# Kernel optimization log

Measured on AMD Instinct MI355X. Metric: run time of the kernel, lower is better.

## Reference

```python
import jax, jax.numpy as jnp
import numpy as np

G, N = 1024, 40            # graphs, nodes per graph (complete graphs)
SLOPE = 0.1                # leaky relu negative slope
SMAT_IDX = jnp.array([0, 1, 2, 3, 1, 4, 5, 6, 2, 5, 7, 8, 3, 6, 8, 9])


def setup_inputs() -> dict:
    key = jax.random.key(0)
    ks = jax.random.split(key, 24)

    # --- graph structure: G identical complete graphs of N nodes ---
    ii, jj = np.meshgrid(np.arange(N), np.arange(N), indexing="ij")
    mask = ii != jj
    src_l, dst_l = ii[mask], jj[mask]              # directed edges per graph
    offs = (np.arange(G) * N)[:, None]
    edge_index = np.stack([(src_l[None] + offs).ravel(),
                           (dst_l[None] + offs).ravel()]).astype(np.int64)
    iu, ju = np.triu_indices(N, 1)
    M = iu.shape[0]                                 # 780 undirected edges
    ud_edges = np.stack([iu, ju], 1).astype(np.int64)
    edge_map = np.zeros((N, N), np.int64)
    edge_map[iu, ju] = np.arange(M)
    edge_map[ju, iu] = np.arange(M)

    def w(k, shape, fan_in):
        return jax.random.normal(k, shape, jnp.float32) / np.sqrt(fan_in)

    inp = {
        "x": jax.random.normal(ks[0], (G * N, 16), jnp.float32),
        "edge_index": jnp.asarray(edge_index),
        "ud_edges": jnp.asarray(ud_edges),
        "edge_map": jnp.asarray(edge_map),
        # GCN stack 6->32->32->64
        "Wg0": w(ks[1], (6, 32), 6),   "bg0": jnp.zeros((32,), jnp.float32),
        "Wg1": w(ks[2], (32, 32), 32), "bg1": jnp.zeros((32,), jnp.float32),
        "Wg2": w(ks[3], (32, 64), 32), "bg2": jnp.zeros((64,), jnp.float32),
        # node MLP 64->64->64->10
        "Wn0": w(ks[4], (64, 64), 64), "bn0": jnp.zeros((64,), jnp.float32),
        "Wn1": w(ks[5], (64, 64), 64), "bn1": jnp.zeros((64,), jnp.float32),
        "Wn2": w(ks[6], (64, 10), 64), "bn2": jnp.zeros((10,), jnp.float32),
        # edge MLP 64->64->64->10
        "We0": w(ks[7], (64, 64), 64), "be0": jnp.zeros((64,), jnp.float32),
        "We1": w(ks[8], (64, 64), 64), "be1": jnp.zeros((64,), jnp.float32),
        "We2": w(ks[9], (64, 10), 64), "be2": jnp.zeros((10,), jnp.float32),
    }
    return inp


def _forward(x, edge_index, ud_edges, edge_map,
             Wg0, bg0, Wg1, bg1, Wg2, bg2,
             Wn0, bn0, Wn1, bn1, Wn2, bn2,
             We0, be0, We1, be1, We2, be2):
    num_nodes = x.shape[0]
    h = x[:, :6]                                   # node_feature_mode == 1
    src, dst = edge_index[0], edge_index[1]

    # GCN normalization (add_self_loops=False, edge_weight=1)
    deg = jax.ops.segment_sum(jnp.ones(src.shape[0], x.dtype), dst,
                              num_segments=num_nodes)
    dis = jnp.where(deg > 0, jax.lax.rsqrt(jnp.maximum(deg, 1e-12)), 0.0)
    norm = dis[src] * dis[dst]                     # [E]

    def gcn(h, W, b):
        m = (h @ W)[src] * norm[:, None]
        return jax.ops.segment_sum(m, dst, num_segments=num_nodes) + b

    # eval mode: dropout is identity
    h = jax.nn.leaky_relu(gcn(h, Wg0, bg0), SLOPE)
    h = jax.nn.leaky_relu(gcn(h, Wg1, bg1), SLOPE)
    h = gcn(h, Wg2, bg2)                           # [G*N, 64]

    hg = h.reshape(G, N, -1)                       # [G, N, 64]

    def mlp(z, Ws, bs):
        for W, b in zip(Ws[:-1], bs[:-1]):
            z = jax.nn.leaky_relu(z @ W + b, SLOPE)
        return z @ Ws[-1] + bs[-1]

    vp = mlp(hg, [Wn0, Wn1, Wn2], [bn0, bn1, bn2])            # [G, N, 10]
    e = hg[:, ud_edges[:, 0], :] + hg[:, ud_edges[:, 1], :]   # [G, M, 64]
    ep = mlp(e, [We0, We1, We2], [be0, be1, be2])             # [G, M, 10]

    # recover_X: diag blocks smat(vp[i]), off-diag smat(ep[edge_map[i,j]])
    epm = ep[:, edge_map, :]                                  # [G, N, N, 10]
    eye = jnp.eye(N, dtype=bool)[None, :, :, None]
    vecs = jnp.where(eye, vp[:, :, None, :], epm)             # [G, N, N, 10]
    blocks = vecs[..., SMAT_IDX].reshape(G, N, N, 4, 4)
    X = blocks.transpose(0, 1, 3, 2, 4).reshape(G, 4 * N, 4 * N)
    return h, X


def reference(x, edge_index, ud_edges, edge_map,
              Wg0, bg0, Wg1, bg1, Wg2, bg2,
              Wn0, bn0, Wn1, bn1, Wn2, bn2,
              We0, be0, We1, be1, We2, be2):
    return _forward(x, edge_index, ud_edges, edge_map,
                    Wg0, bg0, Wg1, bg1, Wg2, bg2,
                    Wn0, bn0, Wn1, bn1, Wn2, bn2,
                    We0, be0, We1, be1, We2, be2)
```

## Files before the change

kernel.cpp:

```cpp
#include <hip/hip_runtime.h>

#define G_GRAPHS 1024
#define N_NODES  40
#define M_EDGES  780
#define NUM_NODES (G_GRAPHS * N_NODES)
#define H_ELEMS  (NUM_NODES * 64)
#define X_STRIDE 160
#define X_PER_G  25600
#define SLOPE 0.1f

#define PACK_PER_MLP 9216

typedef __bf16 bf16x8 __attribute__((ext_vector_type(8)));
typedef unsigned short us8 __attribute__((ext_vector_type(8)));
typedef float f32x4 __attribute__((ext_vector_type(4)));

__device__ __forceinline__ float lrelu(float v) { return fmaxf(v, SLOPE * v); }
__device__ __forceinline__ unsigned short f2bf(float x) {
    __bf16 b = (__bf16)x;
    return __builtin_bit_cast(unsigned short, b);
}
__device__ __forceinline__ unsigned int pk2bf(float a, float b) {
    return (unsigned int)f2bf(a) | ((unsigned int)f2bf(b) << 16);
}

__global__ __launch_bounds__(256) void k_prep(const float* __restrict__ We0,
                                              const float* __restrict__ We1,
                                              const float* __restrict__ We2,
                                              const float* __restrict__ Wn0,
                                              const float* __restrict__ Wn1,
                                              const float* __restrict__ Wn2,
                                              unsigned short* __restrict__ wp) {
    int t = blockIdx.x * 256 + threadIdx.x;
    int mlp = t / PACK_PER_MLP;
    int o = t - mlp * PACK_PER_MLP;
    const float* W0 = mlp ? Wn0 : We0;
    const float* W1 = mlp ? Wn1 : We1;
    const float* W2 = mlp ? Wn2 : We2;
    float val;
    if (o < 8192) {
        const float* W = (o < 4096) ? W0 : W1;
        int idx = o & 4095;
        int j = idx & 7, l = (idx >> 3) & 63, tt = idx >> 9;
        int kt = tt & 1, mt = tt >> 1;
        int k = kt * 32 + ((l >> 4) & 3) * 8 + j;
        int m = mt * 16 + (l & 15);
        val = W[k * 64 + m];
    } else {
        int idx = o - 8192;
        int j = idx & 7, l = (idx >> 3) & 63, kt = idx >> 9;
        int k = kt * 32 + ((l >> 4) & 3) * 8 + j;
        int m = l & 15;
        val = (m < 10) ? W2[k * 10 + m] : 0.f;
    }
    wp[mlp * PACK_PER_MLP + o] = f2bf(val);
}

struct ChunkRegs {
    bf16x8 A1[4][2];
    bf16x8 A2[4][2];
    bf16x8 A3[2];
    float4 bv0[4];
    float4 bv1[4];
    float  bz[4];
};

__device__ __forceinline__ void run_pair(int R0A, int R0B, int w, int l,
                                         const float4* sh4,
                                         unsigned short* sBA,
                                         unsigned short* sBB,
                                         float* sEP,
                                         const ChunkRegs& cr) {
    const int nl = l & 15;
    const int rq = (l >> 4) & 3;
    const int rl = l >> 1;
    const int hf2 = l & 1;

    auto decode = [&](int row, int& ii, int& jj, bool& is_e, bool& is_n) {
        is_e = (row < 780);
        is_n = (row >= 800 && row < 840);
        ii = 0; jj = 0;
        if (is_e) {
            float tq = 6241.0f - 8.0f * (float)row;
            int i0 = (int)(0.5f * (79.0f - sqrtf(tq)));
            i0 = min(38, max(0, i0));
            int cum = 39 * i0 - ((i0 * (i0 - 1)) >> 1);
            if (cum > row) { --i0; cum = 39 * i0 - ((i0 * (i0 - 1)) >> 1); }
            else if (row - cum >= 39 - i0) { cum += 39 - i0; ++i0; }
            ii = i0; jj = i0 + 1 + (row - cum);
        } else if (is_n) {
            ii = jj = row - 800;
        }
    };
    int iiA, jjA, iiB, jjB; bool ieA, inA, ieB, inB;
    decode(R0A + rl, iiA, jjA, ieA, inA);
    decode(R0B + rl, iiB, jjB, ieB, inB);

    auto ebuild = [&](unsigned short* sB, int ii, int jj, bool is_e) {
        unsigned short tmp[32];
#pragma unroll
        for (int q = 0; q < 8; q++) {
            int u = hf2 * 8 + q;
            float4 a = sh4[ii * 16 + (u ^ ((ii & 7) << 1))];
            if (is_e) {
                float4 bq = sh4[jj * 16 + (u ^ ((jj & 7) << 1))];
                a.x += bq.x; a.y += bq.y; a.z += bq.z; a.w += bq.w;
            }
            tmp[4 * q + 0] = f2bf(a.x); tmp[4 * q + 1] = f2bf(a.y);
            tmp[4 * q + 2] = f2bf(a.z); tmp[4 * q + 3] = f2bf(a.w);
        }
        int r_sb = 32 * w + rl;
#pragma unroll
        for (int q = 0; q < 4; q++) {
            int cs = (hf2 * 4 + q) ^ (r_sb & 7);
            *(us8*)((char*)sB + r_sb * 128 + cs * 16) = *(const us8*)(tmp + 8 * q);
        }
    };
    ebuild(sBA, iiA, jjA, ieA);
    ebuild(sBB, iiB, jjB, ieB);

    auto ZB = [&](const unsigned short* s, int nt, int kt) -> bf16x8 {
        int node = 32 * w + nt * 16 + nl;
        int cs = (kt * 4 + rq) ^ (node & 7);
        return __builtin_bit_cast(bf16x8,
            *(const us8*)((const char*)s + node * 128 + cs * 16));
    };
    auto zstore = [&](unsigned short* s, int mt, int nt, const f32x4& v) {
        int node = 32 * w + nt * 16 + nl;
        int cs = (mt * 2 + (rq >> 1)) ^ (node & 7);
        uint2 u = make_uint2(pk2bf(v[0], v[1]), pk2bf(v[2], v[3]));
        *(uint2*)((char*)s + node * 128 + cs * 16 + (rq & 1) * 8) = u;
    };

    auto gemm_layer = [&](unsigned short* s, const bf16x8 A[4][2],
                          const float4* bv) {
        bf16x8 B[2][2];
#pragma unroll
        for (int nt = 0; nt < 2; nt++)
#pragma unroll
            for (int kt = 0; kt < 2; kt++) B[nt][kt] = ZB(s, nt, kt);
#pragma unroll
        for (int mt = 0; mt < 4; mt++) {
            float4 b = bv[mt];
#pragma unroll
            for (int nt = 0; nt < 2; nt++) {
                f32x4 acc = (f32x4){0.f, 0.f, 0.f, 0.f};
                acc = __builtin_amdgcn_mfma_f32_16x16x32_bf16(A[mt][0], B[nt][0], acc, 0, 0, 0);
                acc = __builtin_amdgcn_mfma_f32_16x16x32_bf16(A[mt][1], B[nt][1], acc, 0, 0, 0);
                f32x4 z;
                z[0] = lrelu(acc[0] + b.x); z[1] = lrelu(acc[1] + b.y);
                z[2] = lrelu(acc[2] + b.z); z[3] = lrelu(acc[3] + b.w);
                zstore(s, mt, nt, z);
            }
        }
    };

    gemm_layer(sBA, cr.A1, cr.bv0);
    gemm_layer(sBB, cr.A1, cr.bv0);
    gemm_layer(sBA, cr.A2, cr.bv1);
    gemm_layer(sBB, cr.A2, cr.bv1);

    auto gemm3 = [&](unsigned short* s, int R0) {
        bf16x8 B[2][2];
#pragma unroll
        for (int nt = 0; nt < 2; nt++)
#pragma unroll
            for (int kt = 0; kt < 2; kt++) B[nt][kt] = ZB(s, nt, kt);
#pragma unroll
        for (int nt = 0; nt < 2; nt++) {
            f32x4 acc = (f32x4){0.f, 0.f, 0.f, 0.f};
            acc = __builtin_amdgcn_mfma_f32_16x16x32_bf16(cr.A3[0], B[nt][0], acc, 0, 0, 0);
            acc = __builtin_amdgcn_mfma_f32_16x16x32_bf16(cr.A3[1], B[nt][1], acc, 0, 0, 0);
            int rowe = R0 + nt * 16 + nl;
            bool valid = (rowe < 780) || (rowe >= 800 && rowe < 840);
            if (valid && rq < 3) {
                int epr = (rowe < 780) ? rowe : rowe - 20;
                float* p = sEP + epr * 10 + rq * 4;
                *(float2*)p = make_float2(acc[0] + cr.bz[0], acc[1] + cr.bz[1]);
                if (rq < 2)
                    *(float2*)(p + 2) = make_float2(acc[2] + cr.bz[2], acc[3] + cr.bz[3]);
            }
        }
    };
    gemm3(sBA, R0A);
    gemm3(sBB, R0B);
}

__global__ __launch_bounds__(256, 2) void k_fused(const float* __restrict__ x,
                                                  const float* __restrict__ Wg0,
                                                  const float* __restrict__ bg0,
                                                  const float* __restrict__ Wg1,
                                                  const float* __restrict__ bg1,
                                                  const float* __restrict__ Wg2,
                                                  const float* __restrict__ bg2,
                                                  const unsigned short* __restrict__ wp,
                                                  const float* __restrict__ be0,
                                                  const float* __restrict__ be1,
                                                  const float* __restrict__ be2,
                                                  const float* __restrict__ bn0,
                                                  const float* __restrict__ bn1,
                                                  const float* __restrict__ bn2,
                                                  float* __restrict__ hout,
                                                  float* __restrict__ X) {
    __shared__ __align__(16) char smem[75808];
    float* sh           = (float*)smem;
    unsigned short* sBA = (unsigned short*)(smem + 10240);
    unsigned short* sBB = (unsigned short*)(smem + 26624);
    float* sEP          = (float*)(smem + 43008);
    float* h0  = (float*)smem;
    float* P   = (float*)(smem + 1024);
    float* buf = (float*)(smem + 10240);
    float* h1  = (float*)(smem + 20480);
    float* S   = (float*)(smem + 25600);
    float* h2  = (float*)(smem + 26624);

    const int g = blockIdx.x;
    const int tid = threadIdx.x;
    const int l = tid & 63;
    const int w = tid >> 6;
    const float inv39 = 1.0f / 39.0f;
    const int c32 = tid & 31;
    const int c64 = tid & 63;
    const int rq = (l >> 4) & 3;

    {
        float w0c[6], w1c[32], w2c[32];
#pragma unroll
        for (int f = 0; f < 6; f++)  w0c[f] = Wg0[f * 32 + c32];
#pragma unroll
        for (int m = 0; m < 32; m++) w1c[m] = Wg1[m * 32 + c32];
#pragma unroll
        for (int m = 0; m < 32; m++) w2c[m] = Wg2[m * 64 + c64];
        const float b0c = bg0[c32];
        const float b1c = bg1[c32];
        const float b2c = bg2[c64];

        for (int idx = tid; idx < N_NODES * 6; idx += 256) {
            int n = idx / 6, f = idx - n * 6;
            h0[idx] = x[(g * N_NODES + n) * 16 + f];
        }
        __syncthreads();

        {
            int n0 = tid >> 5;
#pragma unroll
            for (int t = 0; t < 5; t++) {
                int n = n0 + 8 * t;
                float s = 0.f;
#pragma unroll
                for (int f = 0; f < 6; f++) s += h0[n * 6 + f] * w0c[f];
                buf[n * 32 + c32] = s;
            }
        }
        __syncthreads();
        { int grp = tid >> 5; float s = 0.f;
#pragma unroll
          for (int n = grp * 5; n < grp * 5 + 5; n++) s += buf[n * 32 + c32];
          P[grp * 32 + c32] = s; }
        __syncthreads();
        if (tid < 32) { float s = 0.f;
#pragma unroll
          for (int grp = 0; grp < 8; grp++) s += P[grp * 32 + tid];
          S[tid] = s; }
        __syncthreads();
        for (int idx = tid; idx < N_NODES * 32; idx += 256)
            h1[idx] = lrelu((S[c32] - buf[idx]) * inv39 + b0c);
        __syncthreads();

        {
            int n0 = tid >> 5;
#pragma unroll
            for (int t = 0; t < 5; t++) {
                int n = n0 + 8 * t;
                const float4* hp = (const float4*)(h1 + n * 32);
                float s = 0.f;
#pragma unroll
                for (int q = 0; q < 8; q++) {
                    float4 hv = hp[q];
                    s += hv.x * w1c[4 * q + 0] + hv.y * w1c[4 * q + 1]
                       + hv.z * w1c[4 * q + 2] + hv.w * w1c[4 * q + 3];
                }
                buf[n * 32 + c32] = s;
            }
        }
        __syncthreads();
        { int grp = tid >> 5; float s = 0.f;
#pragma unroll
          for (int n = grp * 5; n < grp * 5 + 5; n++) s += buf[n * 32 + c32];
          P[grp * 32 + c32] = s; }
        __syncthreads();
        if (tid < 32) { float s = 0.f;
#pragma unroll
          for (int grp = 0; grp < 8; grp++) s += P[grp * 32 + tid];
          S[tid] = s; }
        __syncthreads();
        for (int idx = tid; idx < N_NODES * 32; idx += 256)
            h2[idx] = lrelu((S[c32] - buf[idx]) * inv39 + b1c);
        __syncthreads();

        {
            int n0 = tid >> 6;
#pragma unroll
            for (int t = 0; t < 10; t++) {
                int n = n0 + 4 * t;
                const float4* hp = (const float4*)(h2 + n * 32);
                float s = 0.f;
#pragma unroll
                for (int q = 0; q < 8; q++) {
                    float4 hv = hp[q];
                    s += hv.x * w2c[4 * q + 0] + hv.y * w2c[4 * q + 1]
                       + hv.z * w2c[4 * q + 2] + hv.w * w2c[4 * q + 3];
                }
                buf[n * 64 + c64] = s;
            }
        }
        __syncthreads();
        { int grp = tid >> 6; float s = 0.f;
#pragma unroll
          for (int n = grp * 10; n < grp * 10 + 10; n++) s += buf[n * 64 + c64];
          P[grp * 64 + c64] = s; }
        __syncthreads();
        if (tid < 64) { float s = 0.f;
#pragma unroll
          for (int grp = 0; grp < 4; grp++) s += P[grp * 64 + tid];
          S[tid] = s; }
        __syncthreads();

        for (int idx = tid; idx < N_NODES * 64; idx += 256) {
            float v = (S[c64] - buf[idx]) * inv39 + b2c;
            hout[g * N_NODES * 64 + idx] = v;
            int n = idx >> 6;
            int u = c64 >> 2;
            int us = u ^ ((n & 7) << 1);
            sh[n * 64 + us * 4 + (c64 & 3)] = v;
        }
    }
    __syncthreads();

    const float4* sh4 = (const float4*)sh;

    auto WA = [&](const unsigned short* base, int mt, int kt) -> bf16x8 {
        return __builtin_bit_cast(bf16x8,
            *(const us8*)(base + ((mt * 2 + kt) * 64 + l) * 8));
    };
    auto loadW = [&](ChunkRegs& cr, const unsigned short* wb,
                     const float* B0, const float* B1, const float* B2) {
#pragma unroll
        for (int mt = 0; mt < 4; mt++) {
#pragma unroll
            for (int kt = 0; kt < 2; kt++) {
                cr.A1[mt][kt] = WA(wb, mt, kt);
                cr.A2[mt][kt] = WA(wb + 4096, mt, kt);
            }
            cr.bv0[mt] = *(const float4*)(B0 + mt * 16 + rq * 4);
            cr.bv1[mt] = *(const float4*)(B1 + mt * 16 + rq * 4);
        }
        cr.A3[0] = WA(wb + 8192, 0, 0);
        cr.A3[1] = WA(wb + 8192, 0, 1);
#pragma unroll
        for (int k = 0; k < 4; k++) {
            int f = rq * 4 + k;
            cr.bz[k] = (f < 10) ? B2[f] : 0.f;
        }
    };

    ChunkRegs ce;
    loadW(ce, wp, be0, be1, be2);

    for (int p = w; p < 14; p += 4) {
        int c1, c2;
        if (p < 12)       { c1 = 2 * p; c2 = 2 * p + 1; }
        else if (p == 12) { c1 = 24;    c2 = 27;        }
        else              { c1 = 25;    c2 = 26;
                            loadW(ce, wp + PACK_PER_MLP, bn0, bn1, bn2); }
        run_pair(32 * c1, 32 * c2, w, l, sh4, sBA, sBB, sEP, ce);
    }

    __syncthreads();

    float* Xg = X + g * X_PER_G;
#pragma unroll
    for (int k = 0; k < 7; k++) {
        int b = k * 256 + tid;
        if (b < 1600) {
            int bi = b / 40;
            int bj = b - bi * 40;
            int ridx;
            if (bi == bj) {
                ridx = 780 + bi;
            } else {
                int mn = min(bi, bj), mx = max(bi, bj);
                ridx = 39 * mn - ((mn * (mn - 1)) >> 1) + (mx - mn - 1);
            }
            const float* ep = sEP + ridx * 10;
            float2 e0 = *(const float2*)(ep + 0);
            float2 e1 = *(const float2*)(ep + 2);
            float2 e2 = *(const float2*)(ep + 4);
            float2 e3 = *(const float2*)(ep + 6);
            float2 e4 = *(const float2*)(ep + 8);
            float f0 = e0.x, f1 = e0.y, f2 = e1.x, f3 = e1.y;
            float f4 = e2.x, f5 = e2.y, f6 = e3.x, f7 = e3.y;
            float f8 = e4.x, f9 = e4.y;
            float4 r0 = make_float4(f0, f1, f2, f3);
            float4 r1 = make_float4(f1, f4, f5, f6);
            float4 r2 = make_float4(f2, f5, f7, f8);
            float4 r3 = make_float4(f3, f6, f8, f9);
            float* p = Xg + (4 * bi) * X_STRIDE + 4 * bj;
            *(float4*)(p + 0 * X_STRIDE) = r0;
            *(float4*)(p + 1 * X_STRIDE) = r1;
            *(float4*)(p + 2 * X_STRIDE) = r2;
            *(float4*)(p + 3 * X_STRIDE) = r3;
        }
    }
}

extern "C" void kernel_launch(void* const* d_in, const int* in_sizes, int n_in,
                              void* d_out, int out_size, void* d_ws, size_t ws_size,
                              hipStream_t stream) {
    const float* x   = (const float*)d_in[0];
    const float* Wg0 = (const float*)d_in[4];
    const float* bg0 = (const float*)d_in[5];
    const float* Wg1 = (const float*)d_in[6];
    const float* bg1 = (const float*)d_in[7];
    const float* Wg2 = (const float*)d_in[8];
    const float* bg2 = (const float*)d_in[9];
    const float* Wn0 = (const float*)d_in[10];
    const float* bn0 = (const float*)d_in[11];
    const float* Wn1 = (const float*)d_in[12];
    const float* bn1 = (const float*)d_in[13];
    const float* Wn2 = (const float*)d_in[14];
    const float* bn2 = (const float*)d_in[15];
    const float* We0 = (const float*)d_in[16];
    const float* be0 = (const float*)d_in[17];
    const float* We1 = (const float*)d_in[18];
    const float* be1 = (const float*)d_in[19];
    const float* We2 = (const float*)d_in[20];
    const float* be2 = (const float*)d_in[21];

    float* hout = (float*)d_out;
    float* X    = hout + H_ELEMS;
    unsigned short* wp = (unsigned short*)d_ws;

    k_prep<<<72, 256, 0, stream>>>(We0, We1, We2, Wn0, Wn1, Wn2, wp);
    k_fused<<<G_GRAPHS, 256, 0, stream>>>(x, Wg0, bg0, Wg1, bg1, Wg2, bg2,
                                          wp, be0, be1, be2, bn0, bn1, bn2,
                                          hout, X);
}
```

Measured before the change: 209.6 us.

## Precompute edge index table, fold bias into MFMA accumulator, drop reduction barriers

Builds a shared-memory lookup table of (i,j) node pairs for the 780 edges once per block, replacing a per-row sqrt-based decode inside the MLP loop. It also initialises the MFMA accumulators with the bias so the separate bias adds disappear. The GCN column-sum reductions are now done redundantly by every thread rather than by a few threads writing to shared memory, which removes one barrier per layer. The cost is a little more shared memory, slightly more redundant LDS reads per thread, and the partial-sum buffer moving to another offset.

```diff
diff --git a/kernel.cpp b/kernel.cpp
--- a/kernel.cpp
+++ b/kernel.cpp
@@ -70,6 +70,7 @@
                                          unsigned short* sBA,
                                          unsigned short* sBB,
                                          float* sEP,
+                                         const unsigned short* sIJ,
                                          const ChunkRegs& cr) {
     const int nl = l & 15;
     const int rq = (l >> 4) & 3;
@@ -81,13 +82,8 @@
         is_n = (row >= 800 && row < 840);
         ii = 0; jj = 0;
         if (is_e) {
-            float tq = 6241.0f - 8.0f * (float)row;
-            int i0 = (int)(0.5f * (79.0f - sqrtf(tq)));
-            i0 = min(38, max(0, i0));
-            int cum = 39 * i0 - ((i0 * (i0 - 1)) >> 1);
-            if (cum > row) { --i0; cum = 39 * i0 - ((i0 * (i0 - 1)) >> 1); }
-            else if (row - cum >= 39 - i0) { cum += 39 - i0; ++i0; }
-            ii = i0; jj = i0 + 1 + (row - cum);
+            unsigned short e = sIJ[row];
+            ii = e >> 8; jj = e & 255;
         } else if (is_n) {
             ii = jj = row - 800;
         }
@@ -144,12 +140,12 @@
             float4 b = bv[mt];
 #pragma unroll
             for (int nt = 0; nt < 2; nt++) {
-                f32x4 acc = (f32x4){0.f, 0.f, 0.f, 0.f};
+                f32x4 acc = (f32x4){b.x, b.y, b.z, b.w};
                 acc = __builtin_amdgcn_mfma_f32_16x16x32_bf16(A[mt][0], B[nt][0], acc, 0, 0, 0);
                 acc = __builtin_amdgcn_mfma_f32_16x16x32_bf16(A[mt][1], B[nt][1], acc, 0, 0, 0);
                 f32x4 z;
-                z[0] = lrelu(acc[0] + b.x); z[1] = lrelu(acc[1] + b.y);
-                z[2] = lrelu(acc[2] + b.z); z[3] = lrelu(acc[3] + b.w);
+                z[0] = lrelu(acc[0]); z[1] = lrelu(acc[1]);
+                z[2] = lrelu(acc[2]); z[3] = lrelu(acc[3]);
                 zstore(s, mt, nt, z);
             }
         }
@@ -168,7 +164,7 @@
             for (int kt = 0; kt < 2; kt++) B[nt][kt] = ZB(s, nt, kt);
 #pragma unroll
         for (int nt = 0; nt < 2; nt++) {
-            f32x4 acc = (f32x4){0.f, 0.f, 0.f, 0.f};
+            f32x4 acc = (f32x4){cr.bz[0], cr.bz[1], cr.bz[2], cr.bz[3]};
             acc = __builtin_amdgcn_mfma_f32_16x16x32_bf16(cr.A3[0], B[nt][0], acc, 0, 0, 0);
             acc = __builtin_amdgcn_mfma_f32_16x16x32_bf16(cr.A3[1], B[nt][1], acc, 0, 0, 0);
             int rowe = R0 + nt * 16 + nl;
@@ -176,9 +172,9 @@
             if (valid && rq < 3) {
                 int epr = (rowe < 780) ? rowe : rowe - 20;
                 float* p = sEP + epr * 10 + rq * 4;
-                *(float2*)p = make_float2(acc[0] + cr.bz[0], acc[1] + cr.bz[1]);
+                *(float2*)p = make_float2(acc[0], acc[1]);
                 if (rq < 2)
-                    *(float2*)(p + 2) = make_float2(acc[2] + cr.bz[2], acc[3] + cr.bz[3]);
+                    *(float2*)(p + 2) = make_float2(acc[2], acc[3]);
             }
         }
     };
@@ -202,17 +198,17 @@
                                                   const float* __restrict__ bn2,
                                                   float* __restrict__ hout,
                                                   float* __restrict__ X) {
-    __shared__ __align__(16) char smem[75808];
+    __shared__ __align__(16) char smem[77408];
     float* sh           = (float*)smem;
     unsigned short* sBA = (unsigned short*)(smem + 10240);
     unsigned short* sBB = (unsigned short*)(smem + 26624);
     float* sEP          = (float*)(smem + 43008);
+    unsigned short* sIJ = (unsigned short*)(smem + 75808);
     float* h0  = (float*)smem;
-    float* P   = (float*)(smem + 1024);
     float* buf = (float*)(smem + 10240);
     float* h1  = (float*)(smem + 20480);
-    float* S   = (float*)(smem + 25600);
     float* h2  = (float*)(smem + 26624);
+    float* P   = (float*)(smem + 43008);
 
     const int g = blockIdx.x;
     const int tid = threadIdx.x;
@@ -223,6 +219,17 @@
     const int c64 = tid & 63;
     const int rq = (l >> 4) & 3;
 
+    for (int m = tid; m < 780; m += 256) {
+        float tq = 6241.0f - 8.0f * (float)m;
+        int i0 = (int)(0.5f * (79.0f - sqrtf(tq)));
+        i0 = min(38, max(0, i0));
+        int cum = 39 * i0 - ((i0 * (i0 - 1)) >> 1);
+        if (cum > m) { --i0; cum = 39 * i0 - ((i0 * (i0 - 1)) >> 1); }
+        else if (m - cum >= 39 - i0) { cum += 39 - i0; ++i0; }
+        int jj = i0 + 1 + (m - cum);
+        sIJ[m] = (unsigned short)((i0 << 8) | jj);
+    }
+
     {
         float w0c[6], w1c[32], w2c[32];
 #pragma unroll
@@ -258,13 +265,11 @@
           for (int n = grp * 5; n < grp * 5 + 5; n++) s += buf[n * 32 + c32];
           P[grp * 32 + c32] = s; }
         __syncthreads();
-        if (tid < 32) { float s = 0.f;
-#pragma unroll
-          for (int grp = 0; grp < 8; grp++) s += P[grp * 32 + tid];
-          S[tid] = s; }
-        __syncthreads();
-        for (int idx = tid; idx < N_NODES * 32; idx += 256)
-            h1[idx] = lrelu((S[c32] - buf[idx]) * inv39 + b0c);
+        { float s0 = 0.f;
+#pragma unroll
+          for (int grp = 0; grp < 8; grp++) s0 += P[grp * 32 + c32];
+          for (int idx = tid; idx < N_NODES * 32; idx += 256)
+              h1[idx] = lrelu((s0 - buf[idx]) * inv39 + b0c); }
         __syncthreads();
 
         {
@@ -289,13 +294,11 @@
           for (int n = grp * 5; n < grp * 5 + 5; n++) s += buf[n * 32 + c32];
           P[grp * 32 + c32] = s; }
         __syncthreads();
-        if (tid < 32) { float s = 0.f;
-#pragma unroll
-          for (int grp = 0; grp < 8; grp++) s += P[grp * 32 + tid];
-          S[tid] = s; }
-        __syncthreads();
-        for (int idx = tid; idx < N_NODES * 32; idx += 256)
-            h2[idx] = lrelu((S[c32] - buf[idx]) * inv39 + b1c);
+        { float s0 = 0.f;
+#pragma unroll
+          for (int grp = 0; grp < 8; grp++) s0 += P[grp * 32 + c32];
+          for (int idx = tid; idx < N_NODES * 32; idx += 256)
+              h2[idx] = lrelu((s0 - buf[idx]) * inv39 + b1c); }
         __syncthreads();
 
         {
@@ -320,20 +323,18 @@
           for (int n = grp * 10; n < grp * 10 + 10; n++) s += buf[n * 64 + c64];
           P[grp * 64 + c64] = s; }
         __syncthreads();
-        if (tid < 64) { float s = 0.f;
-#pragma unroll
-          for (int grp = 0; grp < 4; grp++) s += P[grp * 64 + tid];
-          S[tid] = s; }
-        __syncthreads();
-
-        for (int idx = tid; idx < N_NODES * 64; idx += 256) {
-            float v = (S[c64] - buf[idx]) * inv39 + b2c;
-            hout[g * N_NODES * 64 + idx] = v;
-            int n = idx >> 6;
-            int u = c64 >> 2;
-            int us = u ^ ((n & 7) << 1);
-            sh[n * 64 + us * 4 + (c64 & 3)] = v;
-        }
+
+        { float s0 = 0.f;
+#pragma unroll
+          for (int grp = 0; grp < 4; grp++) s0 += P[grp * 64 + c64];
+          for (int idx = tid; idx < N_NODES * 64; idx += 256) {
+              float v = (s0 - buf[idx]) * inv39 + b2c;
+              hout[g * N_NODES * 64 + idx] = v;
+              int n = idx >> 6;
+              int u = c64 >> 2;
+              int us = u ^ ((n & 7) << 1);
+              sh[n * 64 + us * 4 + (c64 & 3)] = v;
+          } }
     }
     __syncthreads();
 
@@ -373,7 +374,7 @@
         else if (p == 12) { c1 = 24;    c2 = 27;        }
         else              { c1 = 25;    c2 = 26;
                             loadW(ce, wp + PACK_PER_MLP, bn0, bn1, bn2); }
-        run_pair(32 * c1, 32 * c2, w, l, sh4, sBA, sBB, sEP, ce);
+        run_pair(32 * c1, 32 * c2, w, l, sh4, sBA, sBB, sEP, sIJ, ce);
     }
 
     __syncthreads();
```

Result: no change. 209.0 us (-0.3%).
